# Performance work log

Measured on AMD Instinct MI355X. Metric: run time of the kernel, lower is better.

## Reference

```python
import jax, jax.numpy as jnp
import numpy as np

D_MODEL = 1024
N_HEAD = 16
HEAD_SIZE = D_MODEL // N_HEAD
SEQ = 2048
BATCH = 4
LN_EPS = 1e-5


def layer_norm(x, gamma, beta):
    mu = jnp.mean(x, axis=-1, keepdims=True)
    var = jnp.var(x, axis=-1, keepdims=True)
    return (x - mu) * jax.lax.rsqrt(var + LN_EPS) * gamma + beta


def setup_inputs() -> dict:
    key = jax.random.key(0)
    ks = jax.random.split(key, 12)
    s = 0.02
    return {
        "x": jax.random.normal(ks[0], (BATCH, SEQ, D_MODEL), jnp.float32),
        "Wq": jax.random.normal(ks[1], (N_HEAD, D_MODEL, HEAD_SIZE), jnp.float32) * s,
        "Wk": jax.random.normal(ks[2], (N_HEAD, D_MODEL, HEAD_SIZE), jnp.float32) * s,
        "Wv": jax.random.normal(ks[3], (N_HEAD, D_MODEL, HEAD_SIZE), jnp.float32) * s,
        "Wo": jax.random.normal(ks[4], (D_MODEL, D_MODEL), jnp.float32) * s,
        "bo": jnp.zeros((D_MODEL,), jnp.float32),
        "W1": jax.random.normal(ks[5], (D_MODEL, 4 * D_MODEL), jnp.float32) * s,
        "b1": jnp.zeros((4 * D_MODEL,), jnp.float32),
        "W2": jax.random.normal(ks[6], (4 * D_MODEL, D_MODEL), jnp.float32) * s,
        "b2": jnp.zeros((D_MODEL,), jnp.float32),
        "g1": jnp.ones((D_MODEL,), jnp.float32),
        "be1": jnp.zeros((D_MODEL,), jnp.float32),
        "g2": jnp.ones((D_MODEL,), jnp.float32),
        "be2": jnp.zeros((D_MODEL,), jnp.float32),
    }


def reference(x, Wq, Wk, Wv, Wo, bo, W1, b1, W2, b2, g1, be1, g2, be2):
    B, T, C = x.shape
    # --- self-attention branch (dropout = eval identity) ---
    h = layer_norm(x, g1, be1)
    q = jnp.einsum('btc,hcs->bhts', h, Wq)
    k = jnp.einsum('btc,hcs->bhts', h, Wk)
    v = jnp.einsum('btc,hcs->bhts', h, Wv)
    wei = jnp.einsum('bhts,bhus->bhtu', q, k) * (HEAD_SIZE ** -0.5)
    # non-standard diagonal mask: scores on the diagonal are set to 0 (not -inf)
    diag = jnp.eye(T, dtype=bool)
    wei = jnp.where(diag, jnp.zeros((), wei.dtype), wei)
    wei = jax.nn.softmax(wei, axis=-1)
    att = jnp.einsum('bhtu,bhus->bhts', wei, v)          # [B,H,T,hs]
    att = att.transpose(0, 2, 1, 3).reshape(B, T, C)      # concat heads
    sa = att @ Wo + bo
    x = x + sa
    # --- feed-forward branch ---
    h2 = layer_norm(x, g2, be2)
    ff = jax.nn.gelu(h2 @ W1 + b1, approximate=False) @ W2 + b2
    return x + ff
```

## Files before the change

### kernel.cpp

```cpp
#include <hip/hip_runtime.h>
#include <hip/hip_bf16.h>
#include <math.h>

#define D_MODEL 1024
#define N_HEAD 16
#define HEAD 64
#define SEQ 2048
#define BATCH 4
#define ROWS (BATCH*SEQ)
#define FFD 4096

typedef __bf16 bf16;
typedef __attribute__((ext_vector_type(8))) __bf16 bf16x8;
typedef __attribute__((ext_vector_type(4))) __bf16 bf16x4;
typedef __attribute__((ext_vector_type(4))) float f32x4;
typedef __attribute__((ext_vector_type(4))) short short4v;

static_assert(sizeof(bf16x8) == 16, "bf16x8 must be 16B");

__device__ __forceinline__ void async_copy16(const void* g, void* l) {
  __builtin_amdgcn_global_load_lds((const __attribute__((address_space(1))) void*)g,
                                   (__attribute__((address_space(3))) void*)l, 16, 0, 0);
}

__device__ __forceinline__ f32x4 mfma16(bf16x8 a, bf16x8 b, f32x4 c) {
  return __builtin_amdgcn_mfma_f32_16x16x32_bf16(a, b, c, 0, 0, 0);
}

__device__ __forceinline__ f32x4 mfma16k16(bf16x4 a, bf16x4 b, f32x4 c) {
#if __has_builtin(__builtin_amdgcn_mfma_f32_16x16x16_bf16)
  return __builtin_amdgcn_mfma_f32_16x16x16_bf16(a, b, c, 0, 0, 0);
#else
  return __builtin_amdgcn_mfma_f32_16x16x16bf16_1k(__builtin_bit_cast(short4v, a),
                                                   __builtin_bit_cast(short4v, b), c, 0, 0, 0);
#endif
}

__device__ __forceinline__ float fast_exp2(float x) {
#if __has_builtin(__builtin_amdgcn_exp2f)
  return __builtin_amdgcn_exp2f(x);
#else
  float r; asm("v_exp_f32 %0, %1" : "=v"(r) : "v"(x)); return r;
#endif
}

__device__ __forceinline__ float fast_gelu(float x) {
  const float y = 0.7978845608f * (x + 0.044715f * x * x * x);
  const float e = fast_exp2(y * 2.88539008178f);
  return 0.5f * x * (1.f + (1.f - 2.f / (e + 1.f)));
}

__global__ __launch_bounds__(256) void transpose_cast_kernel(const float* __restrict__ in,
                                                             bf16* __restrict__ out,
                                                             int R, int C) {
  __shared__ float ts[32][33];
  const int r0 = blockIdx.y * 32, c0 = blockIdx.x * 32;
  const int t = threadIdx.x, lr = t >> 3, lc = (t & 7) * 4;
  const float4 v = *(const float4*)(in + (size_t)(r0 + lr) * C + c0 + lc);
  ts[lr][lc + 0] = v.x; ts[lr][lc + 1] = v.y; ts[lr][lc + 2] = v.z; ts[lr][lc + 3] = v.w;
  __syncthreads();
  bf16x4 o;
  o[0] = (bf16)ts[lc + 0][lr]; o[1] = (bf16)ts[lc + 1][lr];
  o[2] = (bf16)ts[lc + 2][lr]; o[3] = (bf16)ts[lc + 3][lr];
  *(bf16x4*)(out + (size_t)(c0 + lr) * R + r0 + lc) = o;
}

__global__ __launch_bounds__(256) void qkv_transpose_kernel(const float* __restrict__ Wq,
                                                            const float* __restrict__ Wk,
                                                            const float* __restrict__ Wv,
                                                            bf16* __restrict__ out) {
  __shared__ float ts[32][33];
  const int mat = blockIdx.z / N_HEAD, h = blockIdx.z % N_HEAD;
  const float* W = (mat == 0 ? Wq : mat == 1 ? Wk : Wv) + (size_t)h * D_MODEL * HEAD;
  bf16* o = out + (size_t)mat * D_MODEL * D_MODEL + (size_t)(h * HEAD) * D_MODEL;
  const int c0 = blockIdx.x * 32, s0 = blockIdx.y * 32;
  const int t = threadIdx.x, lr = t >> 3, lc = (t & 7) * 4;
  const float4 v = *(const float4*)(W + (size_t)(c0 + lr) * HEAD + s0 + lc);
  ts[lr][lc + 0] = v.x; ts[lr][lc + 1] = v.y; ts[lr][lc + 2] = v.z; ts[lr][lc + 3] = v.w;
  __syncthreads();
  bf16x4 ov;
  ov[0] = (bf16)ts[lc + 0][lr]; ov[1] = (bf16)ts[lc + 1][lr];
  ov[2] = (bf16)ts[lc + 2][lr]; ov[3] = (bf16)ts[lc + 3][lr];
  *(bf16x4*)(o + (size_t)(s0 + lr) * D_MODEL + c0 + lc) = ov;
}

__global__ __launch_bounds__(256) void ln_kernel(const float* __restrict__ x,
                                                 const float* __restrict__ g,
                                                 const float* __restrict__ b,
                                                 bf16* __restrict__ h) {
  const int row = blockIdx.x, t = threadIdx.x;
  const float4 v = *(const float4*)(x + (size_t)row * D_MODEL + t * 4);
  float s = v.x + v.y + v.z + v.w;
  float ss = v.x * v.x + v.y * v.y + v.z * v.z + v.w * v.w;
#pragma unroll
  for (int m = 1; m < 64; m <<= 1) { s += __shfl_xor(s, m); ss += __shfl_xor(ss, m); }
  __shared__ float red[8];
  const int wave = t >> 6, lane = t & 63;
  if (lane == 0) { red[wave] = s; red[4 + wave] = ss; }
  __syncthreads();
  s = red[0] + red[1] + red[2] + red[3];
  ss = red[4] + red[5] + red[6] + red[7];
  const float mu = s * (1.f / D_MODEL);
  const float rstd = rsqrtf(ss * (1.f / D_MODEL) - mu * mu + 1e-5f);
  const float4 gv = *(const float4*)(g + t * 4);
  const float4 bv = *(const float4*)(b + t * 4);
  bf16x4 o;
  o[0] = (bf16)((v.x - mu) * rstd * gv.x + bv.x);
  o[1] = (bf16)((v.y - mu) * rstd * gv.y + bv.y);
  o[2] = (bf16)((v.z - mu) * rstd * gv.z + bv.z);
  o[3] = (bf16)((v.w - mu) * rstd * gv.w + bv.w);
  *(bf16x4*)(h + (size_t)row * D_MODEL + t * 4) = o;
}

#define STAGE_A(kt2, h)                                                          \
  do {                                                                           \
    const int off_ = (kt2) * 64 + (h) * 32;                                      \
    bf16* d_ = aDst0 + (((kt2) & 1) * 2 + (h)) * AHALF;                          \
    async_copy16(aSrc0 + off_, d_);                                              \
    if (ASTEPS == 2) async_copy16(aSrc1 + off_, d_ + 4096);                      \
  } while (0)

#define STAGE_B(kt2, h)                                                          \
  do {                                                                           \
    const int off_ = (kt2) * 64 + (h) * 32;                                      \
    bf16* d_ = bDst0 + (((kt2) & 1) * 2 + (h)) * 8192;                           \
    async_copy16(bSrc0 + off_, d_);                                              \
    async_copy16(bSrc1 + off_, d_ + 4096);                                       \
  } while (0)

template <int EPI, int BM>
__device__ __forceinline__ void gemm_body(const bf16* A, const bf16* Bt, int K,
                                          void* outp, const float* bias,
                                          const float* resid, bf16* q_out,
                                          bf16* k_out, bf16* vt_out, int N) {
  constexpr int ASTEPS = BM / 128;
  constexpr int MPW = BM / 2;
  constexpr int MREP = MPW / 16;
  constexpr int AHALF = BM * 32;
  __shared__ bf16 As[2 * 2 * BM * 32];
  __shared__ bf16 Bs[2 * 2 * 256 * 32];
  const int t = threadIdx.x, wave = t >> 6, lane = t & 63;
  const int l15 = lane & 15, l4 = lane >> 4;
  const int lin = ((int)blockIdx.x & 7) * ((int)gridDim.x >> 3) + ((int)blockIdx.x >> 3);
  const int nbn = N >> 8;
  const int bn = lin % nbn, bm = lin / nbn;
  const int nk = K >> 6;

  const int sc = (lane & 3) ^ ((lane >> 3) & 3);
  const int r0 = wave * 16 + (lane >> 2);
  const bf16* aSrc0 = A + (size_t)(bm * BM + r0) * K + sc * 8;
  const bf16* aSrc1 = (ASTEPS == 2) ? (A + (size_t)(bm * BM + 128 + r0) * K + sc * 8) : aSrc0;
  const bf16* bSrc0 = Bt + (size_t)(bn * 256 + r0) * K + sc * 8;
  const bf16* bSrc1 = Bt + (size_t)(bn * 256 + 128 + r0) * K + sc * 8;
  bf16* aDst0 = As + wave * 512;
  bf16* bDst0 = Bs + wave * 512;

  const int wm = wave >> 2, wn = wave & 3;
  const int rw = wm * MPW, cw = wn * 64;
  const int pc = (l4 ^ ((l15 >> 1) & 3)) * 8;

  f32x4 acc[MREP][4];
#pragma unroll
  for (int mi = 0; mi < MREP; mi++)
#pragma unroll
    for (int ni = 0; ni < 4; ni++) { f32x4 z = {0.f, 0.f, 0.f, 0.f}; acc[mi][ni] = z; }

  STAGE_A(0, 0); STAGE_B(0, 0); STAGE_A(0, 1); STAGE_B(0, 1);
  STAGE_A(1, 0); STAGE_B(1, 0); STAGE_A(1, 1);
  if constexpr (ASTEPS == 2) asm volatile("s_waitcnt vmcnt(6)" ::: "memory");
  else                       asm volatile("s_waitcnt vmcnt(4)" ::: "memory");
  __builtin_amdgcn_s_barrier();
  __builtin_amdgcn_sched_barrier(0);

  for (int kt = 0; kt < nk; kt++) {
    const bf16* Ab = As + (kt & 1) * (2 * AHALF);
    const bf16* Bb = Bs + (kt & 1) * (2 * 8192);
    bf16x8 aF[MREP], b0, b1;

#pragma unroll
    for (int mi = 0; mi < MREP; mi++)
      aF[mi] = *(const bf16x8*)(Ab + (rw + mi * 16 + l15) * 32 + pc);
    b0 = *(const bf16x8*)(Bb + (cw + l15) * 32 + pc);
    b1 = *(const bf16x8*)(Bb + (cw + 16 + l15) * 32 + pc);
    if (kt + 1 < nk) STAGE_B(kt + 1, 1);
    __builtin_amdgcn_s_barrier();
    asm volatile("s_waitcnt lgkmcnt(0)" ::: "memory");
    __builtin_amdgcn_s_setprio(1);
#pragma unroll
    for (int mi = 0; mi < MREP; mi++) {
      acc[mi][0] = mfma16(aF[mi], b0, acc[mi][0]);
      acc[mi][1] = mfma16(aF[mi], b1, acc[mi][1]);
    }
    __builtin_amdgcn_s_setprio(0);
    __builtin_amdgcn_s_barrier();

    b0 = *(const bf16x8*)(Bb + (cw + 32 + l15) * 32 + pc);
    b1 = *(const bf16x8*)(Bb + (cw + 48 + l15) * 32 + pc);
    if (kt + 2 < nk) STAGE_A(kt + 2, 0);
    __builtin_amdgcn_s_barrier();
    asm volatile("s_waitcnt lgkmcnt(0)" ::: "memory");
    __builtin_amdgcn_s_setprio(1);
#pragma unroll
    for (int mi = 0; mi < MREP; mi++) {
      acc[mi][2] = mfma16(aF[mi], b0, acc[mi][2]);
      acc[mi][3] = mfma16(aF[mi], b1, acc[mi][3]);
    }
    __builtin_amdgcn_s_setprio(0);
    __builtin_amdgcn_s_barrier();

#pragma unroll
    for (int mi = 0; mi < MREP; mi++)
      aF[mi] = *(const bf16x8*)(Ab + AHALF + (rw + mi * 16 + l15) * 32 + pc);
    b0 = *(const bf16x8*)(Bb + 8192 + (cw + l15) * 32 + pc);
    b1 = *(const bf16x8*)(Bb + 8192 + (cw + 16 + l15) * 32 + pc);
    if (kt + 2 < nk) STAGE_B(kt + 2, 0);
    __builtin_amdgcn_s_barrier();
    asm volatile("s_waitcnt lgkmcnt(0)" ::: "memory");
    __builtin_amdgcn_s_setprio(1);
#pragma unroll
    for (int mi = 0; mi < MREP; mi++) {
      acc[mi][0] = mfma16(aF[mi], b0, acc[mi][0]);
      acc[mi][1] = mfma16(aF[mi], b1, acc[mi][1]);
    }
    __builtin_amdgcn_s_setprio(0);
    __builtin_amdgcn_s_barrier();

    b0 = *(const bf16x8*)(Bb + 8192 + (cw + 32 + l15) * 32 + pc);
    b1 = *(const bf16x8*)(Bb + 8192 + (cw + 48 + l15) * 32 + pc);
    if (kt + 2 < nk) {
      STAGE_A(kt + 2, 1);
      if constexpr (ASTEPS == 2) asm volatile("s_waitcnt vmcnt(6)" ::: "memory");
      else                       asm volatile("s_waitcnt vmcnt(4)" ::: "memory");
    } else {
      asm volatile("s_waitcnt vmcnt(0)" ::: "memory");
    }
    __builtin_amdgcn_s_barrier();
    asm volatile("s_waitcnt lgkmcnt(0)" ::: "memory");
    __builtin_amdgcn_s_setprio(1);
#pragma unroll
    for (int mi = 0; mi < MREP; mi++) {
      acc[mi][2] = mfma16(aF[mi], b0, acc[mi][2]);
      acc[mi][3] = mfma16(aF[mi], b1, acc[mi][3]);
    }
    __builtin_amdgcn_s_setprio(0);
    __builtin_amdgcn_s_barrier();
    __builtin_amdgcn_sched_barrier(0);
  }

#pragma unroll
  for (int mi = 0; mi < MREP; mi++) {
#pragma unroll
    for (int ni = 0; ni < 4; ni++) {
      const int n = bn * 256 + cw + ni * 16 + l15;
#pragma unroll
      for (int e = 0; e < 4; e++) {
        const int m = bm * BM + rw + mi * 16 + l4 * 4 + e;
        float val = acc[mi][ni][e];
        if constexpr (EPI == 0) {
          const int b = m >> 11, tt = m & 2047;
          if (n < D_MODEL) {
            const int hh = n >> 6, sgl = n & 63;
            q_out[(size_t)((b * N_HEAD + hh) * SEQ + tt) * HEAD + sgl] = (bf16)val;
          } else if (n < 2 * D_MODEL) {
            const int n2 = n - D_MODEL, hh = n2 >> 6, sgl = n2 & 63;
            k_out[(size_t)((b * N_HEAD + hh) * SEQ + tt) * HEAD + sgl] = (bf16)val;
          } else {
            const int n2 = n - 2 * D_MODEL, hh = n2 >> 6, sgl = n2 & 63;
            vt_out[(size_t)((b * N_HEAD + hh) * HEAD + sgl) * SEQ + tt] = (bf16)val;
          }
        } else if constexpr (EPI == 1) {
          ((float*)outp)[(size_t)m * N + n] = val + bias[n] + resid[(size_t)m * N + n];
        } else if constexpr (EPI == 2) {
          ((bf16*)outp)[(size_t)m * N + n] = (bf16)fast_gelu(val + bias[n]);
        } else {
          ((float*)outp)[(size_t)m * N + n] = val + bias[n] + resid[(size_t)m * N + n];
        }
      }
    }
  }
}

#undef STAGE_A
#undef STAGE_B

__global__ __launch_bounds__(512, 2) void gemm_qkv_kernel(const bf16* __restrict__ A,
                                                          const bf16* __restrict__ Bt,
                                                          bf16* __restrict__ q_out,
                                                          bf16* __restrict__ k_out,
                                                          bf16* __restrict__ vt_out) {
  gemm_body<0, 256>(A, Bt, D_MODEL, nullptr, nullptr, nullptr, q_out, k_out, vt_out, 3 * D_MODEL);
}

__global__ __launch_bounds__(512, 2) void gemm_proj_kernel(const bf16* __restrict__ A,
                                                           const bf16* __restrict__ Bt,
                                                           float* __restrict__ outp,
                                                           const float* __restrict__ bias,
                                                           const float* __restrict__ resid) {
  gemm_body<1, 128>(A, Bt, D_MODEL, outp, bias, resid, nullptr, nullptr, nullptr, D_MODEL);
}

__global__ __launch_bounds__(512, 2) void gemm_ff1_kernel(const bf16* __restrict__ A,
                                                          const bf16* __restrict__ Bt,
                                                          bf16* __restrict__ outp,
                                                          const float* __restrict__ bias) {
  gemm_body<2, 256>(A, Bt, D_MODEL, outp, bias, nullptr, nullptr, nullptr, nullptr, FFD);
}

__global__ __launch_bounds__(512, 2) void gemm_ff2_kernel(const bf16* __restrict__ A,
                                                          const bf16* __restrict__ Bt,
                                                          float* __restrict__ outp,
                                                          const float* __restrict__ bias,
                                                          const float* __restrict__ resid) {
  gemm_body<3, 128>(A, Bt, FFD, outp, bias, resid, nullptr, nullptr, nullptr, D_MODEL);
}

__global__ __launch_bounds__(256, 2) void attn_kernel(const bf16* __restrict__ q,
                                                      const bf16* __restrict__ k,
                                                      const bf16* __restrict__ vt,
                                                      bf16* __restrict__ att) {
  __shared__ bf16 Ks[64 * 64];
  __shared__ bf16 Vs[64 * 64];
  const int t = threadIdx.x, wave = t >> 6, lane = t & 63;
  const int l15 = lane & 15, l4 = lane >> 4;
  const int bh = blockIdx.x & 63, qblk = blockIdx.x >> 6;
  const bf16* qb = q + (size_t)bh * SEQ * HEAD;
  const bf16* kb = k + (size_t)bh * SEQ * HEAD;
  const bf16* vb = vt + (size_t)bh * HEAD * SEQ;
  const int qrow = qblk * 256 + wave * 64;

  const int tr = t >> 3, tc = t & 7, sw = tc ^ (tr & 7);
  const bf16* ksrc0 = kb + (size_t)tr * HEAD + sw * 8;
  const bf16* ksrc1 = kb + (size_t)(tr + 32) * HEAD + sw * 8;
  const bf16* vsrc0 = vb + (size_t)tr * SEQ + sw * 8;
  const bf16* vsrc1 = vb + (size_t)(tr + 32) * SEQ + sw * 8;
  bf16* kd0 = Ks + t * 8; bf16* kd1 = Ks + t * 8 + 2048;
  bf16* vd0 = Vs + t * 8; bf16* vd1 = Vs + t * 8 + 2048;

  const float qscale = 0.125f * 1.44269504088896340736f;
  bf16x8 qf[4][2];
#pragma unroll
  for (int qs = 0; qs < 4; qs++)
#pragma unroll
    for (int h = 0; h < 2; h++) {
      const bf16x8 raw = *(const bf16x8*)(qb + (size_t)(qrow + qs * 16 + l15) * HEAD + h * 32 + l4 * 8);
      bf16x8 sc;
#pragma unroll
      for (int e = 0; e < 8; e++) sc[e] = (bf16)((float)raw[e] * qscale);
      qf[qs][h] = sc;
    }

  f32x4 o[4][4];
  float lsum[4] = {0.f, 0.f, 0.f, 0.f};
#pragma unroll
  for (int qs = 0; qs < 4; qs++)
#pragma unroll
    for (int dm = 0; dm < 4; dm++) { f32x4 z = {0.f, 0.f, 0.f, 0.f}; o[qs][dm] = z; }

  const int rsw = l15 & 7;

  for (int u0 = 0; u0 < SEQ; u0 += 64) {
    __syncthreads();
    async_copy16(ksrc0 + (size_t)u0 * HEAD, kd0);
    async_copy16(ksrc1 + (size_t)u0 * HEAD, kd1);
    async_copy16(vsrc0 + u0, vd0);
    async_copy16(vsrc1 + u0, vd1);
    __syncthreads();

    bf16x8 kf[4][2];
#pragma unroll
    for (int n = 0; n < 4; n++)
#pragma unroll
      for (int h = 0; h < 2; h++)
        kf[n][h] = *(const bf16x8*)(Ks + (n * 16 + l15) * 64 + (((h << 2) | l4) ^ rsw) * 8);
    bf16x4 vf[4][4];
#pragma unroll
    for (int dm = 0; dm < 4; dm++)
#pragma unroll
      for (int n = 0; n < 4; n++)
        vf[dm][n] = *(const bf16x4*)(Vs + (dm * 16 + l15) * 64 + ((((n << 1) | (l4 >> 1)) ^ rsw) * 8) + (l4 & 1) * 4);

#pragma unroll
    for (int qs = 0; qs < 4; qs++) {
      f32x4 s[4];
#pragma unroll
      for (int n = 0; n < 4; n++) {
        f32x4 c = {0.f, 0.f, 0.f, 0.f};
        c = mfma16(kf[n][0], qf[qs][0], c);
        c = mfma16(kf[n][1], qf[qs][1], c);
        s[n] = c;
      }
      if (u0 == qrow) {
#pragma unroll
        for (int r = 0; r < 4; r++)
          s[qs][r] = (l15 == l4 * 4 + r) ? 0.f : s[qs][r];
      }
      bf16x4 pf[4];
      float ls = 0.f;
#pragma unroll
      for (int n = 0; n < 4; n++) {
        f32x4 pv;
#pragma unroll
        for (int r = 0; r < 4; r++) { pv[r] = fast_exp2(s[n][r]); ls += pv[r]; }
        bf16x4 pb;
#pragma unroll
        for (int r = 0; r < 4; r++) pb[r] = (bf16)pv[r];
        pf[n] = pb;
      }
      lsum[qs] += ls;
#pragma unroll
      for (int dm = 0; dm < 4; dm++) {
        f32x4 acc = o[qs][dm];
#pragma unroll
        for (int n = 0; n < 4; n++) acc = mfma16k16(vf[dm][n], pf[n], acc);
        o[qs][dm] = acc;
      }
    }
  }

#pragma unroll
  for (int qs = 0; qs < 4; qs++) {
    float l = lsum[qs];
    l += __shfl_xor(l, 16);
    l += __shfl_xor(l, 32);
    lsum[qs] = l;
  }
  const int b = bh >> 4, hh = bh & 15;
#pragma unroll
  for (int qs = 0; qs < 4; qs++) {
    const float linv = 1.0f / lsum[qs];
#pragma unroll
    for (int dm = 0; dm < 4; dm++) {
      bf16x4 ov;
#pragma unroll
      for (int r = 0; r < 4; r++) ov[r] = (bf16)(o[qs][dm][r] * linv);
      *(bf16x4*)(att + (size_t)(b * SEQ + qrow + qs * 16 + l15) * D_MODEL + hh * HEAD + dm * 16 + l4 * 4) = ov;
    }
  }
}

extern "C" void kernel_launch(void* const* d_in, const int* in_sizes, int n_in,
                              void* d_out, int out_size, void* d_ws, size_t ws_size,
                              hipStream_t stream) {
  const float* x   = (const float*)d_in[0];
  const float* Wq  = (const float*)d_in[1];
  const float* Wk  = (const float*)d_in[2];
  const float* Wv  = (const float*)d_in[3];
  const float* Wo  = (const float*)d_in[4];
  const float* bo  = (const float*)d_in[5];
  const float* W1  = (const float*)d_in[6];
  const float* b1  = (const float*)d_in[7];
  const float* W2  = (const float*)d_in[8];
  const float* b2  = (const float*)d_in[9];
  const float* g1  = (const float*)d_in[10];
  const float* be1 = (const float*)d_in[11];
  const float* g2  = (const float*)d_in[12];
  const float* be2 = (const float*)d_in[13];
  float* out = (float*)d_out;

  bf16* Wqkv_t = (bf16*)d_ws;
  bf16* Wo_t   = Wqkv_t + (size_t)3 * D_MODEL * D_MODEL;
  bf16* W1_t   = Wo_t + (size_t)D_MODEL * D_MODEL;
  bf16* W2_t   = W1_t + (size_t)FFD * D_MODEL;
  bf16* hbuf   = W2_t + (size_t)D_MODEL * FFD;
  float* x1    = (float*)(hbuf + (size_t)ROWS * D_MODEL);
  bf16* big    = (bf16*)(x1 + (size_t)ROWS * D_MODEL);
  bf16* qbuf   = big;
  bf16* kbuf   = qbuf + (size_t)ROWS * D_MODEL;
  bf16* vtbuf  = kbuf + (size_t)ROWS * D_MODEL;
  bf16* ffbuf  = big;
  bf16* attb   = big + (size_t)ROWS * FFD;

  qkv_transpose_kernel<<<dim3(D_MODEL / 32, HEAD / 32, 3 * N_HEAD), 256, 0, stream>>>(Wq, Wk, Wv, Wqkv_t);
  transpose_cast_kernel<<<dim3(D_MODEL / 32, D_MODEL / 32), 256, 0, stream>>>(Wo, Wo_t, D_MODEL, D_MODEL);
  transpose_cast_kernel<<<dim3(FFD / 32, D_MODEL / 32), 256, 0, stream>>>(W1, W1_t, D_MODEL, FFD);
  transpose_cast_kernel<<<dim3(D_MODEL / 32, FFD / 32), 256, 0, stream>>>(W2, W2_t, FFD, D_MODEL);
  ln_kernel<<<ROWS, 256, 0, stream>>>(x, g1, be1, hbuf);
  gemm_qkv_kernel<<<dim3((3 * D_MODEL / 256) * (ROWS / 256)), 512, 0, stream>>>(
      hbuf, Wqkv_t, qbuf, kbuf, vtbuf);
  attn_kernel<<<64 * (SEQ / 256), 256, 0, stream>>>(qbuf, kbuf, vtbuf, attb);
  gemm_proj_kernel<<<dim3((D_MODEL / 256) * (ROWS / 128)), 512, 0, stream>>>(
      attb, Wo_t, x1, bo, x);
  ln_kernel<<<ROWS, 256, 0, stream>>>(x1, g2, be2, hbuf);
  gemm_ff1_kernel<<<dim3((FFD / 256) * (ROWS / 256)), 512, 0, stream>>>(
      hbuf, W1_t, ffbuf, b1);
  gemm_ff2_kernel<<<dim3((D_MODEL / 256) * (ROWS / 128)), 512, 0, stream>>>(
      ffbuf, W2_t, out, b2, x1);
}
```

Before: 592.1 us.

## Restructure GEMM main loop to load all B fragments once per k-half

```diff
diff --git a/kernel.cpp b/kernel.cpp
--- a/kernel.cpp
+++ b/kernel.cpp
@@ -21,6 +21,14 @@
 __device__ __forceinline__ void async_copy16(const void* g, void* l) {
   __builtin_amdgcn_global_load_lds((const __attribute__((address_space(1))) void*)g,
                                    (__attribute__((address_space(3))) void*)l, 16, 0, 0);
+}
+
+__device__ __forceinline__ bf16x8 dsr16(const bf16* p) {
+  bf16x8 r;
+  const __attribute__((address_space(3))) bf16* lp =
+      (const __attribute__((address_space(3))) bf16*)(unsigned int)(size_t)p;
+  asm volatile("ds_read_b128 %0, %1" : "=v"(r) : "v"(lp));
+  return r;
 }
 
 __device__ __forceinline__ f32x4 mfma16(bf16x8 a, bf16x8 b, f32x4 c) {
@@ -136,6 +144,7 @@
   constexpr int ASTEPS = BM / 128;
   constexpr int MPW = BM / 2;
   constexpr int MREP = MPW / 16;
+  constexpr int MH = MREP / 2;
   constexpr int AHALF = BM * 32;
   __shared__ bf16 As[2 * 2 * BM * 32];
   __shared__ bf16 Bs[2 * 2 * 256 * 32];
@@ -166,85 +175,78 @@
     for (int ni = 0; ni < 4; ni++) { f32x4 z = {0.f, 0.f, 0.f, 0.f}; acc[mi][ni] = z; }
 
   STAGE_A(0, 0); STAGE_B(0, 0); STAGE_A(0, 1); STAGE_B(0, 1);
-  STAGE_A(1, 0); STAGE_B(1, 0); STAGE_A(1, 1);
+  STAGE_B(1, 0); STAGE_A(1, 0); STAGE_B(1, 1);
   if constexpr (ASTEPS == 2) asm volatile("s_waitcnt vmcnt(6)" ::: "memory");
-  else                       asm volatile("s_waitcnt vmcnt(4)" ::: "memory");
+  else                       asm volatile("s_waitcnt vmcnt(5)" ::: "memory");
   __builtin_amdgcn_s_barrier();
   __builtin_amdgcn_sched_barrier(0);
 
   for (int kt = 0; kt < nk; kt++) {
     const bf16* Ab = As + (kt & 1) * (2 * AHALF);
-    const bf16* Bb = Bs + (kt & 1) * (2 * 8192);
-    bf16x8 aF[MREP], b0, b1;
-
-#pragma unroll
-    for (int mi = 0; mi < MREP; mi++)
-      aF[mi] = *(const bf16x8*)(Ab + (rw + mi * 16 + l15) * 32 + pc);
-    b0 = *(const bf16x8*)(Bb + (cw + l15) * 32 + pc);
-    b1 = *(const bf16x8*)(Bb + (cw + 16 + l15) * 32 + pc);
-    if (kt + 1 < nk) STAGE_B(kt + 1, 1);
+    const bf16* Bb = Bs + (kt & 1) * 16384;
+    bf16x8 aF[MH], bF[4];
+
+    if (kt + 1 < nk) STAGE_A(kt + 1, 1);
+#pragma unroll
+    for (int mi = 0; mi < MH; mi++) aF[mi] = dsr16(Ab + (rw + mi * 16 + l15) * 32 + pc);
+#pragma unroll
+    for (int ni = 0; ni < 4; ni++) bF[ni] = dsr16(Bb + (cw + ni * 16 + l15) * 32 + pc);
+    asm volatile("s_waitcnt lgkmcnt(0)" ::: "memory");
     __builtin_amdgcn_s_barrier();
+    __builtin_amdgcn_sched_barrier(0);
+    __builtin_amdgcn_s_setprio(1);
+#pragma unroll
+    for (int mi = 0; mi < MH; mi++)
+#pragma unroll
+      for (int ni = 0; ni < 4; ni++) acc[mi][ni] = mfma16(aF[mi], bF[ni], acc[mi][ni]);
+    __builtin_amdgcn_s_setprio(0);
+
+    if (kt + 2 < nk) STAGE_B(kt + 2, 0);
+#pragma unroll
+    for (int mi = 0; mi < MH; mi++) aF[mi] = dsr16(Ab + (rw + (MH + mi) * 16 + l15) * 32 + pc);
     asm volatile("s_waitcnt lgkmcnt(0)" ::: "memory");
+    __builtin_amdgcn_s_barrier();
+    __builtin_amdgcn_sched_barrier(0);
     __builtin_amdgcn_s_setprio(1);
 #pragma unroll
-    for (int mi = 0; mi < MREP; mi++) {
-      acc[mi][0] = mfma16(aF[mi], b0, acc[mi][0]);
-      acc[mi][1] = mfma16(aF[mi], b1, acc[mi][1]);
-    }
+    for (int mi = 0; mi < MH; mi++)
+#pragma unroll
+      for (int ni = 0; ni < 4; ni++) acc[MH + mi][ni] = mfma16(aF[mi], bF[ni], acc[MH + mi][ni]);
     __builtin_amdgcn_s_setprio(0);
+
+    if (kt + 2 < nk) STAGE_A(kt + 2, 0);
+#pragma unroll
+    for (int mi = 0; mi < MH; mi++) aF[mi] = dsr16(Ab + AHALF + (rw + mi * 16 + l15) * 32 + pc);
+#pragma unroll
+    for (int ni = 0; ni < 4; ni++) bF[ni] = dsr16(Bb + 8192 + (cw + ni * 16 + l15) * 32 + pc);
+    asm volatile("s_waitcnt lgkmcnt(0)" ::: "memory");
     __builtin_amdgcn_s_barrier();
-
-    b0 = *(const bf16x8*)(Bb + (cw + 32 + l15) * 32 + pc);
-    b1 = *(const bf16x8*)(Bb + (cw + 48 + l15) * 32 + pc);
-    if (kt + 2 < nk) STAGE_A(kt + 2, 0);
-    __builtin_amdgcn_s_barrier();
-    asm volatile("s_waitcnt lgkmcnt(0)" ::: "memory");
+    __builtin_amdgcn_sched_barrier(0);
     __builtin_amdgcn_s_setprio(1);
 #pragma unroll
-    for (int mi = 0; mi < MREP; mi++) {
-      acc[mi][2] = mfma16(aF[mi], b0, acc[mi][2]);
-      acc[mi][3] = mfma16(aF[mi], b1, acc[mi][3]);
-    }
+    for (int mi = 0; mi < MH; mi++)
+#pragma unroll
+      for (int ni = 0; ni < 4; ni++) acc[mi][ni] = mfma16(aF[mi], bF[ni], acc[mi][ni]);
     __builtin_amdgcn_s_setprio(0);
-    __builtin_amdgcn_s_barrier();
-
-#pragma unroll
-    for (int mi = 0; mi < MREP; mi++)
-      aF[mi] = *(const bf16x8*)(Ab + AHALF + (rw + mi * 16 + l15) * 32 + pc);
-    b0 = *(const bf16x8*)(Bb + 8192 + (cw + l15) * 32 + pc);
-    b1 = *(const bf16x8*)(Bb + 8192 + (cw + 16 + l15) * 32 + pc);
-    if (kt + 2 < nk) STAGE_B(kt + 2, 0);
-    __builtin_amdgcn_s_barrier();
-    asm volatile("s_waitcnt lgkmcnt(0)" ::: "memory");
-    __builtin_amdgcn_s_setprio(1);
-#pragma unroll
-    for (int mi = 0; mi < MREP; mi++) {
-      acc[mi][0] = mfma16(aF[mi], b0, acc[mi][0]);
-      acc[mi][1] = mfma16(aF[mi], b1, acc[mi][1]);
-    }
-    __builtin_amdgcn_s_setprio(0);
-    __builtin_amdgcn_s_barrier();
-
-    b0 = *(const bf16x8*)(Bb + 8192 + (cw + 32 + l15) * 32 + pc);
-    b1 = *(const bf16x8*)(Bb + 8192 + (cw + 48 + l15) * 32 + pc);
+
+    if (kt + 2 < nk) STAGE_B(kt + 2, 1);
+#pragma unroll
+    for (int mi = 0; mi < MH; mi++) aF[mi] = dsr16(Ab + AHALF + (rw + (MH + mi) * 16 + l15) * 32 + pc);
     if (kt + 2 < nk) {
-      STAGE_A(kt + 2, 1);
       if constexpr (ASTEPS == 2) asm volatile("s_waitcnt vmcnt(6)" ::: "memory");
-      else                       asm volatile("s_waitcnt vmcnt(4)" ::: "memory");
+      else                       asm volatile("s_waitcnt vmcnt(5)" ::: "memory");
     } else {
       asm volatile("s_waitcnt vmcnt(0)" ::: "memory");
     }
-    __builtin_amdgcn_s_barrier();
     asm volatile("s_waitcnt lgkmcnt(0)" ::: "memory");
-    __builtin_amdgcn_s_setprio(1);
-#pragma unroll
-    for (int mi = 0; mi < MREP; mi++) {
-      acc[mi][2] = mfma16(aF[mi], b0, acc[mi][2]);
-      acc[mi][3] = mfma16(aF[mi], b1, acc[mi][3]);
-    }
-    __builtin_amdgcn_s_setprio(0);
     __builtin_amdgcn_s_barrier();
     __builtin_amdgcn_sched_barrier(0);
+    __builtin_amdgcn_s_setprio(1);
+#pragma unroll
+    for (int mi = 0; mi < MH; mi++)
+#pragma unroll
+      for (int ni = 0; ni < 4; ni++) acc[MH + mi][ni] = mfma16(aF[mi], bF[ni], acc[MH + mi][ni]);
+    __builtin_amdgcn_s_setprio(0);
   }
 
 #pragma unroll
@@ -288,7 +290,7 @@
                                                           bf16* __restrict__ q_out,
                                                           bf16* __restrict__ k_out,
                                                           bf16* __restrict__ vt_out) {
-  gemm_body<0, 256>(A, Bt, D_MODEL, nullptr, nullptr, nullptr, q_out, k_out, vt_out, 3 * D_MODEL);
+  gemm_body<0, 128>(A, Bt, D_MODEL, nullptr, nullptr, nullptr, q_out, k_out, vt_out, 3 * D_MODEL);
 }
 
 __global__ __launch_bounds__(512, 2) void gemm_proj_kernel(const bf16* __restrict__ A,
@@ -475,7 +477,7 @@
   transpose_cast_kernel<<<dim3(FFD / 32, D_MODEL / 32), 256, 0, stream>>>(W1, W1_t, D_MODEL, FFD);
   transpose_cast_kernel<<<dim3(D_MODEL / 32, FFD / 32), 256, 0, stream>>>(W2, W2_t, FFD, D_MODEL);
   ln_kernel<<<ROWS, 256, 0, stream>>>(x, g1, be1, hbuf);
-  gemm_qkv_kernel<<<dim3((3 * D_MODEL / 256) * (ROWS / 256)), 512, 0, stream>>>(
+  gemm_qkv_kernel<<<dim3((3 * D_MODEL / 256) * (ROWS / 128)), 512, 0, stream>>>(
       hbuf, Wqkv_t, qbuf, kbuf, vtbuf);
   attn_kernel<<<64 * (SEQ / 256), 256, 0, stream>>>(qbuf, kbuf, vtbuf, attb);
   gemm_proj_kernel<<<dim3((D_MODEL / 256) * (ROWS / 128)), 512, 0, stream>>>(
```

Measured after the change: 525.6 us. 11.2% less time.
